# Kernel tuning notes

Measured on AMD Instinct MI355X. Metric: run time of the kernel, lower is better.

## Reference

```python
import jax, jax.numpy as jnp
import numpy as np

B, C, L, E = 65536, 16, 32, 32
EPS = 1e-12

def _normalize(x, axis=-1):
    # F.normalize: x / max(||x||_2, eps)
    n = jnp.sqrt(jnp.sum(x * x, axis=axis, keepdims=True))
    return x / jnp.maximum(n, EPS)

def _linear(x, W, b):
    # torch nn.Linear: y = x @ W.T + b, W: [out, in]
    return jnp.einsum('bcl,el->bce', x, W) + b

def setup_inputs() -> dict:
    key = jax.random.key(0)
    ks = jax.random.split(key, 12)
    s_l = 1.0 / np.sqrt(L)
    s_p1 = 1.0 / np.sqrt(C * E)
    s_p2 = 1.0 / np.sqrt(C * 3)
    return {
        'embed1': jax.random.normal(ks[0], (B, C, L), jnp.float32),
        'embed2': jax.random.normal(ks[1], (B, C, L), jnp.float32),
        'qW': jax.random.uniform(ks[2], (E, L), jnp.float32, -s_l, s_l),
        'qb': jax.random.uniform(ks[3], (E,), jnp.float32, -s_l, s_l),
        'kW': jax.random.uniform(ks[4], (E, L), jnp.float32, -s_l, s_l),
        'kb': jax.random.uniform(ks[5], (E,), jnp.float32, -s_l, s_l),
        'vW': jax.random.uniform(ks[6], (E, L), jnp.float32, -s_l, s_l),
        'vb': jax.random.uniform(ks[7], (E,), jnp.float32, -s_l, s_l),
        'p1W': jax.random.uniform(ks[8], (C * 3, C * E), jnp.float32, -s_p1, s_p1),
        'p1b': jax.random.uniform(ks[9], (C * 3,), jnp.float32, -s_p1, s_p1),
        'p2W': jax.random.uniform(ks[10], (3, C * 3), jnp.float32, -s_p2, s_p2),
        'p2b': jax.random.uniform(ks[11], (3,), jnp.float32, -s_p2, s_p2),
    }

def reference(embed1, embed2, qW, qb, kW, kb, vW, vb, p1W, p1b, p2W, p2b):
    query = _linear(embed1, qW, qb) * _linear(embed2, qW, qb)   # [B,C,E]
    key_t = _linear(embed1, kW, kb) * _linear(embed2, kW, kb)   # [B,C,E]
    value = _linear(embed1, vW, vb) * _linear(embed2, vW, vb)   # [B,C,E]
    attn = jnp.einsum('bce,bde->bcd', _normalize(query), _normalize(key_t))  # [B,C,C]
    # torch F.softmax with dim=None on a 3-D tensor -> legacy dim=0 (batch axis)
    attn = jax.nn.softmax(attn, axis=0)
    # dropout(p=0.2) is identity in eval mode
    out = jnp.einsum('bcd,bce->bde', attn, value)  # attn.transpose(1,2) @ value, [B,C,E]
    h = out.reshape(out.shape[0], -1)              # [B, C*E]
    h = jax.nn.relu(h @ p1W.T + p1b) @ p2W.T + p2b  # [B, 3]
    return _normalize(h)
```

## Files before the change

### kernel.cpp

```cpp
#include <hip/hip_runtime.h>

#define B_TOT 65536
#define WS_P1W 4096
#define WS_EV  (1u << 20)

typedef float f32x4 __attribute__((ext_vector_type(4)));
typedef short s16x8 __attribute__((ext_vector_type(8)));

__device__ __forceinline__ float bf2f(unsigned short h) {
    unsigned u = ((unsigned)h) << 16;
    return __builtin_bit_cast(float, u);
}
__device__ __forceinline__ unsigned pack2(float a, float b) {
    unsigned ua = __builtin_bit_cast(unsigned, a) + 0x8000u;
    unsigned ub = __builtin_bit_cast(unsigned, b) + 0x8000u;
    return __builtin_amdgcn_perm(ub, ua, 0x07060302u);
}
__device__ __forceinline__ unsigned short f2bf(float f) {
    return (unsigned short)((__builtin_bit_cast(unsigned, f) + 0x8000u) >> 16);
}
__device__ __forceinline__ s16x8 cvt8(float4 a, float4 b) {
    uint4 u;
    u.x = pack2(a.x, a.y); u.y = pack2(a.z, a.w);
    u.z = pack2(b.x, b.y); u.w = pack2(b.z, b.w);
    return __builtin_bit_cast(s16x8, u);
}
#define MFMA(a, b, c) __builtin_amdgcn_mfma_f32_16x16x32_bf16((a), (b), (c), 0, 0, 0)

__global__ __launch_bounds__(256) void k0_prep(const float* __restrict__ p1W,
                                               char* __restrict__ ws) {
    int idx = blockIdx.x * 256 + threadIdx.x;
    if (blockIdx.x == 0 && threadIdx.x < 256)
        ((float*)ws)[threadIdx.x] = 0.f;
    int jj   = idx & 7;
    int lane = (idx >> 3) & 63;
    int ktnt = idx >> 9;
    int kt = ktnt & 15, nt = ktnt >> 4;
    int n_lo = lane & 15, q8 = lane >> 4;
    int j  = nt * 16 + n_lo;
    int ip = kt * 32 + q8 * 8 + jj;
    int e_lo = ip >> 5, qq = (ip >> 3) & 3, hh = (ip >> 2) & 1, r = ip & 3;
    int orig = (qq * 4 + r) * 32 + (e_lo + 16 * hh);
    ((unsigned short*)(ws + WS_P1W))[idx] = f2bf(p1W[j * 512 + orig]);
}

__global__ __launch_bounds__(256) void k1_stats(
    const float* __restrict__ e1, const float* __restrict__ e2,
    const float* __restrict__ qW, const float* __restrict__ qb,
    const float* __restrict__ kW, const float* __restrict__ kb,
    const float* __restrict__ vW, const float* __restrict__ vb,
    char* __restrict__ ws) {

    const int tid = threadIdx.x;
    const int lane = tid & 63;
    const int widx = tid >> 6;
    const int col = lane & 15;
    const int quad = lane >> 4;

    __shared__ __align__(16) unsigned short qk_lds[4][2][16 * 40];
    __shared__ float Dblk[256];
    Dblk[tid] = 0.f;
    __syncthreads();

    s16x8 wq[2], wk[2], wv[2];
    f32x4 cbq[2], cbk[2], cbv[2];
    for (int h = 0; h < 2; ++h) {
        int row = col + 16 * h;
        const float4* pq = (const float4*)(qW + row * 32 + quad * 8);
        const float4* pk = (const float4*)(kW + row * 32 + quad * 8);
        const float4* pv = (const float4*)(vW + row * 32 + quad * 8);
        wq[h] = cvt8(pq[0], pq[1]);
        wk[h] = cvt8(pk[0], pk[1]);
        wv[h] = cvt8(pv[0], pv[1]);
        float qv = qb[row], kv = kb[row], vv = vb[row];
        cbq[h] = (f32x4){qv, qv, qv, qv};
        cbk[h] = (f32x4){kv, kv, kv, kv};
        cbv[h] = (f32x4){vv, vv, vv, vv};
    }

    unsigned short* qbuf = qk_lds[widx][0];
    unsigned short* kbuf = qk_lds[widx][1];
    float dacc[4] = {0.f, 0.f, 0.f, 0.f};
    char* evbase = ws + WS_EV;
    const f32x4 z = {0.f, 0.f, 0.f, 0.f};

    const int gw = blockIdx.x * 4 + widx;
    for (int i = 0; i < 8; ++i) {
        const int b = gw * 8 + i;
        const float4* x1p = (const float4*)(e1 + (size_t)b * 512 + col * 32 + quad * 8);
        const float4* x2p = (const float4*)(e2 + (size_t)b * 512 + col * 32 + quad * 8);
        float4 a0 = x1p[0], a1 = x1p[1];
        float4 b0 = x2p[0], b1 = x2p[1];
        s16x8 fx1 = cvt8(a0, a1);
        s16x8 fx2 = cvt8(b0, b1);

        f32x4 q1[2], q2[2], k1[2], k2[2], v1[2], v2[2];
        for (int h = 0; h < 2; ++h) {
            q1[h] = MFMA(fx1, wq[h], cbq[h]); q2[h] = MFMA(fx2, wq[h], cbq[h]);
            k1[h] = MFMA(fx1, wk[h], cbk[h]); k2[h] = MFMA(fx2, wk[h], cbk[h]);
            v1[h] = MFMA(fx1, wv[h], cbv[h]); v2[h] = MFMA(fx2, wv[h], cbv[h]);
        }
        float Qt[2][4], Kt[2][4], Vv[2][4];
        for (int h = 0; h < 2; ++h)
            for (int r = 0; r < 4; ++r) {
                Qt[h][r] = q1[h][r] * q2[h][r];
                Kt[h][r] = k1[h][r] * k2[h][r];
                Vv[h][r] = v1[h][r] * v2[h][r];
            }
        for (int r = 0; r < 4; ++r) {
            int w = (quad * 4 + r) * 20 + col;
            ((unsigned*)qbuf)[w] = pack2(Qt[0][r], Qt[1][r]);
            ((unsigned*)kbuf)[w] = pack2(Kt[0][r], Kt[1][r]);
        }
        s16x8 aq = *(const s16x8*)(qbuf + col * 40 + quad * 8);
        s16x8 bk = *(const s16x8*)(kbuf + col * 40 + quad * 8);
        float qv[8], kv[8], ssq = 0.f, ssk = 0.f;
        for (int j = 0; j < 8; ++j) {
            qv[j] = bf2f((unsigned short)aq[j]); ssq += qv[j] * qv[j];
            kv[j] = bf2f((unsigned short)bk[j]); ssk += kv[j] * kv[j];
        }
        ssq += __shfl_xor(ssq, 16); ssq += __shfl_xor(ssq, 32);
        ssk += __shfl_xor(ssk, 16); ssk += __shfl_xor(ssk, 32);
        float sq = 1.f / fmaxf(sqrtf(ssq), 1e-12f);
        float sk = 1.f / fmaxf(sqrtf(ssk), 1e-12f);
        uint4 uq, uk;
        uq.x = pack2(qv[0] * sq, qv[1] * sq); uq.y = pack2(qv[2] * sq, qv[3] * sq);
        uq.z = pack2(qv[4] * sq, qv[5] * sq); uq.w = pack2(qv[6] * sq, qv[7] * sq);
        uk.x = pack2(kv[0] * sk, kv[1] * sk); uk.y = pack2(kv[2] * sk, kv[3] * sk);
        uk.z = pack2(kv[4] * sk, kv[5] * sk); uk.w = pack2(kv[6] * sk, kv[7] * sk);
        aq = __builtin_bit_cast(s16x8, uq);
        bk = __builtin_bit_cast(s16x8, uk);
        f32x4 S = MFMA(aq, bk, z);

        char* bbase = evbase + (size_t)b * 1536;
        float ex[4];
        for (int r = 0; r < 4; ++r) { ex[r] = __expf(S[r]); dacc[r] += ex[r]; }
        uint2 est; est.x = pack2(ex[0], ex[1]); est.y = pack2(ex[2], ex[3]);
        *(uint2*)(bbase + col * 32 + quad * 8) = est;
        for (int h = 0; h < 2; ++h) {
            uint2 vst;
            vst.x = pack2(Vv[h][0], Vv[h][1]);
            vst.y = pack2(Vv[h][2], Vv[h][3]);
            *(uint2*)(bbase + 512 + ((h * 16 + col) * 2 + (quad >> 1)) * 16 + (quad & 1) * 8) = vst;
        }
    }
    for (int r = 0; r < 4; ++r)
        atomicAdd(&Dblk[col * 16 + quad * 4 + r], dacc[r]);
    __syncthreads();
    atomicAdd(((float*)ws) + tid, Dblk[tid]);
}

__global__ __launch_bounds__(256) void k2_apply(
    const char* __restrict__ ws, const float* __restrict__ p1b,
    const float* __restrict__ p2W, const float* __restrict__ p2b,
    float* __restrict__ out) {

    const int tid = threadIdx.x;
    const int lane = tid & 63;
    const int widx = tid >> 6;
    const int col = lane & 15;
    const int quad = lane >> 4;
    const int qm = quad & 1;

    __shared__ __align__(16) unsigned short Hs[16 * 512];
    float* P = (float*)Hs;

    const float* Dws = (const float*)ws;
    float dinv[8];
    for (int j = 0; j < 8; ++j)
        dinv[j] = 1.f / Dws[col * 16 + qm * 8 + j];

    const char* evbase = ws + WS_EV;
    const unsigned short* p1wp = (const unsigned short*)(ws + WS_P1W);
    const int g = blockIdx.x;
    const f32x4 z = {0.f, 0.f, 0.f, 0.f};
    const s16x8 zz = {0, 0, 0, 0, 0, 0, 0, 0};

    for (int ii = 0; ii < 4; ++ii) {
        const int i = widx * 4 + ii;
        const int b = g * 16 + i;
        const char* bbase = evbase + (size_t)b * 1536;
        s16x8 eraw = *(const s16x8*)(bbase + col * 32 + qm * 16);
        s16x8 bf0 = *(const s16x8*)(bbase + 512 + (col * 2 + qm) * 16);
        s16x8 bf1 = *(const s16x8*)(bbase + 512 + ((16 + col) * 2 + qm) * 16);
        float ef[8];
        for (int j = 0; j < 8; ++j)
            ef[j] = bf2f((unsigned short)eraw[j]) * dinv[j];
        uint4 ua;
        ua.x = pack2(ef[0], ef[1]); ua.y = pack2(ef[2], ef[3]);
        ua.z = pack2(ef[4], ef[5]); ua.w = pack2(ef[6], ef[7]);
        s16x8 afrag = __builtin_bit_cast(s16x8, ua);
        if (quad >= 2) { afrag = zz; bf0 = zz; bf1 = zz; }
        f32x4 o0 = MFMA(afrag, bf0, z);
        f32x4 o1 = MFMA(afrag, bf1, z);
        uint4 uh;
        uh.x = pack2(o0[0], o0[1]); uh.y = pack2(o0[2], o0[3]);
        uh.z = pack2(o1[0], o1[1]); uh.w = pack2(o1[2], o1[3]);
        int chunk = (col * 4 + quad) ^ (i & 7);
        *(uint4*)(Hs + i * 512 + chunk * 8) = uh;
    }
    __syncthreads();

    f32x4 acc[3] = {z, z, z};
    for (int t = 0; t < 4; ++t) {
        int kt = widx * 4 + t;
        int chunk = (kt * 4 + quad) ^ (col & 7);
        s16x8 a = *(const s16x8*)(Hs + col * 512 + chunk * 8);
        for (int nt = 0; nt < 3; ++nt) {
            s16x8 bw = *(const s16x8*)(p1wp + ((nt * 16 + kt) * 64 + lane) * 8);
            acc[nt] = MFMA(a, bw, acc[nt]);
        }
    }
    __syncthreads();

    for (int nt = 0; nt < 3; ++nt)
        *(f32x4*)(P + (widx * 64 + lane) * 12 + nt * 4) = acc[nt];
    __syncthreads();

    if (widx == 0) {
        f32x4 s[3] = {z, z, z};
        for (int w = 0; w < 4; ++w)
            for (int nt = 0; nt < 3; ++nt) {
                f32x4 pv = *(const f32x4*)(P + (w * 64 + lane) * 12 + nt * 4);
                s[nt] += pv;
            }
        float p2w[3][3], p1bias[3];
        for (int nt = 0; nt < 3; ++nt) {
            p1bias[nt] = p1b[col + 16 * nt];
            for (int t = 0; t < 3; ++t) p2w[nt][t] = p2W[t * 48 + col + 16 * nt];
        }
        const float pb0 = p2b[0], pb1 = p2b[1], pb2 = p2b[2];
        float pp[4][3] = {};
        for (int nt = 0; nt < 3; ++nt)
            for (int r = 0; r < 4; ++r) {
                float hv = fmaxf(s[nt][r] + p1bias[nt], 0.f);
                pp[r][0] += hv * p2w[nt][0];
                pp[r][1] += hv * p2w[nt][1];
                pp[r][2] += hv * p2w[nt][2];
            }
        for (int m = 1; m <= 8; m <<= 1)
            for (int r = 0; r < 4; ++r)
                for (int t = 0; t < 3; ++t)
                    pp[r][t] += __shfl_xor(pp[r][t], m);
        for (int r = 0; r < 4; ++r) {
            float h0 = pp[r][0] + pb0, h1 = pp[r][1] + pb1, h2 = pp[r][2] + pb2;
            float inv = 1.f / fmaxf(sqrtf(h0 * h0 + h1 * h1 + h2 * h2), 1e-12f);
            if (col < 3) {
                float v = (col == 0) ? h0 : ((col == 1) ? h1 : h2);
                out[(size_t)(g * 16 + quad * 4 + r) * 3 + col] = v * inv;
            }
        }
    }
}

extern "C" void kernel_launch(void* const* d_in, const int* in_sizes, int n_in,
                              void* d_out, int out_size, void* d_ws, size_t ws_size,
                              hipStream_t stream) {
    const float* e1  = (const float*)d_in[0];
    const float* e2  = (const float*)d_in[1];
    const float* qW  = (const float*)d_in[2];
    const float* qb  = (const float*)d_in[3];
    const float* kW  = (const float*)d_in[4];
    const float* kb  = (const float*)d_in[5];
    const float* vW  = (const float*)d_in[6];
    const float* vb  = (const float*)d_in[7];
    const float* p1W = (const float*)d_in[8];
    const float* p1b = (const float*)d_in[9];
    const float* p2W = (const float*)d_in[10];
    const float* p2b = (const float*)d_in[11];
    float* out = (float*)d_out;
    char* ws = (char*)d_ws;

    k0_prep<<<96, 256, 0, stream>>>(p1W, ws);
    k1_stats<<<2048, 256, 0, stream>>>(e1, e2, qW, qb, kW, kb, vW, vb, ws);
    k2_apply<<<4096, 256, 0, stream>>>(ws, p1b, p2W, p2b, out);
}
```

Before: 342.3 us.

## Replace global atomics with per-block partials, prefetch loads, and split final reduction across warps

```diff
diff --git a/kernel.cpp b/kernel.cpp
--- a/kernel.cpp
+++ b/kernel.cpp
@@ -3,6 +3,8 @@
 #define B_TOT 65536
 #define WS_P1W 4096
 #define WS_EV  (1u << 20)
+#define EV_BYTES 100663296u
+#define WS_PART (WS_EV + EV_BYTES)
 
 typedef float f32x4 __attribute__((ext_vector_type(4)));
 typedef short s16x8 __attribute__((ext_vector_type(8)));
@@ -27,24 +29,7 @@
 }
 #define MFMA(a, b, c) __builtin_amdgcn_mfma_f32_16x16x32_bf16((a), (b), (c), 0, 0, 0)
 
-__global__ __launch_bounds__(256) void k0_prep(const float* __restrict__ p1W,
-                                               char* __restrict__ ws) {
-    int idx = blockIdx.x * 256 + threadIdx.x;
-    if (blockIdx.x == 0 && threadIdx.x < 256)
-        ((float*)ws)[threadIdx.x] = 0.f;
-    int jj   = idx & 7;
-    int lane = (idx >> 3) & 63;
-    int ktnt = idx >> 9;
-    int kt = ktnt & 15, nt = ktnt >> 4;
-    int n_lo = lane & 15, q8 = lane >> 4;
-    int j  = nt * 16 + n_lo;
-    int ip = kt * 32 + q8 * 8 + jj;
-    int e_lo = ip >> 5, qq = (ip >> 3) & 3, hh = (ip >> 2) & 1, r = ip & 3;
-    int orig = (qq * 4 + r) * 32 + (e_lo + 16 * hh);
-    ((unsigned short*)(ws + WS_P1W))[idx] = f2bf(p1W[j * 512 + orig]);
-}
-
-__global__ __launch_bounds__(256) void k1_stats(
+__global__ __launch_bounds__(256, 8) void k1_stats(
     const float* __restrict__ e1, const float* __restrict__ e2,
     const float* __restrict__ qW, const float* __restrict__ qb,
     const float* __restrict__ kW, const float* __restrict__ kb,
@@ -63,7 +48,8 @@
     __syncthreads();
 
     s16x8 wq[2], wk[2], wv[2];
-    f32x4 cbq[2], cbk[2], cbv[2];
+    float bq[2], bk[2], bv[2];
+#pragma unroll
     for (int h = 0; h < 2; ++h) {
         int row = col + 16 * h;
         const float4* pq = (const float4*)(qW + row * 32 + quad * 8);
@@ -72,10 +58,7 @@
         wq[h] = cvt8(pq[0], pq[1]);
         wk[h] = cvt8(pk[0], pk[1]);
         wv[h] = cvt8(pv[0], pv[1]);
-        float qv = qb[row], kv = kb[row], vv = vb[row];
-        cbq[h] = (f32x4){qv, qv, qv, qv};
-        cbk[h] = (f32x4){kv, kv, kv, kv};
-        cbv[h] = (f32x4){vv, vv, vv, vv};
+        bq[h] = qb[row]; bk[h] = kb[row]; bv[h] = vb[row];
     }
 
     unsigned short* qbuf = qk_lds[widx][0];
@@ -85,39 +68,57 @@
     const f32x4 z = {0.f, 0.f, 0.f, 0.f};
 
     const int gw = blockIdx.x * 4 + widx;
+    const float* p1base = e1 + (size_t)gw * 8 * 512 + col * 32 + quad * 8;
+    const float* p2base = e2 + (size_t)gw * 8 * 512 + col * 32 + quad * 8;
+
+    float4 na0 = *(const float4*)(p1base);
+    float4 na1 = *(const float4*)(p1base + 4);
+    float4 nb0 = *(const float4*)(p2base);
+    float4 nb1 = *(const float4*)(p2base + 4);
+
     for (int i = 0; i < 8; ++i) {
         const int b = gw * 8 + i;
-        const float4* x1p = (const float4*)(e1 + (size_t)b * 512 + col * 32 + quad * 8);
-        const float4* x2p = (const float4*)(e2 + (size_t)b * 512 + col * 32 + quad * 8);
-        float4 a0 = x1p[0], a1 = x1p[1];
-        float4 b0 = x2p[0], b1 = x2p[1];
+        float4 a0 = na0, a1 = na1, b0 = nb0, b1 = nb1;
+        if (i < 7) {
+            const float* q1p = p1base + (i + 1) * 512;
+            const float* q2p = p2base + (i + 1) * 512;
+            na0 = *(const float4*)(q1p);
+            na1 = *(const float4*)(q1p + 4);
+            nb0 = *(const float4*)(q2p);
+            nb1 = *(const float4*)(q2p + 4);
+        }
         s16x8 fx1 = cvt8(a0, a1);
         s16x8 fx2 = cvt8(b0, b1);
 
-        f32x4 q1[2], q2[2], k1[2], k2[2], v1[2], v2[2];
+        f32x4 q1v[2], q2v[2], k1v[2], k2v[2], v1v[2], v2v[2];
+#pragma unroll
         for (int h = 0; h < 2; ++h) {
-            q1[h] = MFMA(fx1, wq[h], cbq[h]); q2[h] = MFMA(fx2, wq[h], cbq[h]);
-            k1[h] = MFMA(fx1, wk[h], cbk[h]); k2[h] = MFMA(fx2, wk[h], cbk[h]);
-            v1[h] = MFMA(fx1, wv[h], cbv[h]); v2[h] = MFMA(fx2, wv[h], cbv[h]);
+            q1v[h] = MFMA(fx1, wq[h], z); q2v[h] = MFMA(fx2, wq[h], z);
+            k1v[h] = MFMA(fx1, wk[h], z); k2v[h] = MFMA(fx2, wk[h], z);
+            v1v[h] = MFMA(fx1, wv[h], z); v2v[h] = MFMA(fx2, wv[h], z);
         }
         float Qt[2][4], Kt[2][4], Vv[2][4];
+#pragma unroll
         for (int h = 0; h < 2; ++h)
+#pragma unroll
             for (int r = 0; r < 4; ++r) {
-                Qt[h][r] = q1[h][r] * q2[h][r];
-                Kt[h][r] = k1[h][r] * k2[h][r];
-                Vv[h][r] = v1[h][r] * v2[h][r];
+                Qt[h][r] = (q1v[h][r] + bq[h]) * (q2v[h][r] + bq[h]);
+                Kt[h][r] = (k1v[h][r] + bk[h]) * (k2v[h][r] + bk[h]);
+                Vv[h][r] = (v1v[h][r] + bv[h]) * (v2v[h][r] + bv[h]);
             }
+#pragma unroll
         for (int r = 0; r < 4; ++r) {
             int w = (quad * 4 + r) * 20 + col;
             ((unsigned*)qbuf)[w] = pack2(Qt[0][r], Qt[1][r]);
             ((unsigned*)kbuf)[w] = pack2(Kt[0][r], Kt[1][r]);
         }
         s16x8 aq = *(const s16x8*)(qbuf + col * 40 + quad * 8);
-        s16x8 bk = *(const s16x8*)(kbuf + col * 40 + quad * 8);
+        s16x8 bk8 = *(const s16x8*)(kbuf + col * 40 + quad * 8);
         float qv[8], kv[8], ssq = 0.f, ssk = 0.f;
+#pragma unroll
         for (int j = 0; j < 8; ++j) {
             qv[j] = bf2f((unsigned short)aq[j]); ssq += qv[j] * qv[j];
-            kv[j] = bf2f((unsigned short)bk[j]); ssk += kv[j] * kv[j];
+            kv[j] = bf2f((unsigned short)bk8[j]); ssk += kv[j] * kv[j];
         }
         ssq += __shfl_xor(ssq, 16); ssq += __shfl_xor(ssq, 32);
         ssk += __shfl_xor(ssk, 16); ssk += __shfl_xor(ssk, 32);
@@ -129,14 +130,16 @@
         uk.x = pack2(kv[0] * sk, kv[1] * sk); uk.y = pack2(kv[2] * sk, kv[3] * sk);
         uk.z = pack2(kv[4] * sk, kv[5] * sk); uk.w = pack2(kv[6] * sk, kv[7] * sk);
         aq = __builtin_bit_cast(s16x8, uq);
-        bk = __builtin_bit_cast(s16x8, uk);
-        f32x4 S = MFMA(aq, bk, z);
+        bk8 = __builtin_bit_cast(s16x8, uk);
+        f32x4 S = MFMA(aq, bk8, z);
 
         char* bbase = evbase + (size_t)b * 1536;
         float ex[4];
+#pragma unroll
         for (int r = 0; r < 4; ++r) { ex[r] = __expf(S[r]); dacc[r] += ex[r]; }
         uint2 est; est.x = pack2(ex[0], ex[1]); est.y = pack2(ex[2], ex[3]);
         *(uint2*)(bbase + col * 32 + quad * 8) = est;
+#pragma unroll
         for (int h = 0; h < 2; ++h) {
             uint2 vst;
             vst.x = pack2(Vv[h][0], Vv[h][1]);
@@ -144,10 +147,43 @@
             *(uint2*)(bbase + 512 + ((h * 16 + col) * 2 + (quad >> 1)) * 16 + (quad & 1) * 8) = vst;
         }
     }
+#pragma unroll
     for (int r = 0; r < 4; ++r)
         atomicAdd(&Dblk[col * 16 + quad * 4 + r], dacc[r]);
     __syncthreads();
-    atomicAdd(((float*)ws) + tid, Dblk[tid]);
+    ((float*)(ws + WS_PART))[blockIdx.x * 256 + tid] = Dblk[tid];
+}
+
+__global__ __launch_bounds__(256) void k1b_prep(const float* __restrict__ p1W,
+                                                char* __restrict__ ws) {
+    const int t = threadIdx.x;
+    const int idx = blockIdx.x * 256 + t;
+    if (idx < 24576) {
+        int jj   = idx & 7;
+        int lane = (idx >> 3) & 63;
+        int ktnt = idx >> 9;
+        int kt = ktnt & 15, nt = ktnt >> 4;
+        int n_lo = lane & 15, q8 = lane >> 4;
+        int j2  = nt * 16 + n_lo;
+        int ip  = kt * 32 + q8 * 8 + jj;
+        int e_lo = ip >> 5, qq = (ip >> 3) & 3, hh = (ip >> 2) & 1, r = ip & 3;
+        int orig = (qq * 4 + r) * 32 + (e_lo + 16 * hh);
+        ((unsigned short*)(ws + WS_P1W))[idx] = f2bf(p1W[j2 * 512 + orig]);
+    }
+    const float* part = (const float*)(ws + WS_PART);
+    const int j = blockIdx.x;
+    float s = 0.f;
+#pragma unroll
+    for (int k = 0; k < 8; ++k)
+        s += part[(size_t)(k * 256 + t) * 256 + j];
+    __shared__ float red[256];
+    red[t] = s;
+    __syncthreads();
+    for (int o = 128; o > 0; o >>= 1) {
+        if (t < o) red[t] += red[t + o];
+        __syncthreads();
+    }
+    if (t == 0) ((float*)ws)[j] = 1.f / red[0];
 }
 
 __global__ __launch_bounds__(256) void k2_apply(
@@ -165,10 +201,19 @@
     __shared__ __align__(16) unsigned short Hs[16 * 512];
     float* P = (float*)Hs;
 
+    float p1bias[3], p2w[3][3];
+#pragma unroll
+    for (int nt = 0; nt < 3; ++nt) {
+        p1bias[nt] = p1b[col + 16 * nt];
+#pragma unroll
+        for (int t2 = 0; t2 < 3; ++t2) p2w[nt][t2] = p2W[t2 * 48 + col + 16 * nt];
+    }
+    const float pb0 = p2b[0], pb1 = p2b[1], pb2 = p2b[2];
+
     const float* Dws = (const float*)ws;
-    float dinv[8];
-    for (int j = 0; j < 8; ++j)
-        dinv[j] = 1.f / Dws[col * 16 + qm * 8 + j];
+    const float4 dva = *(const float4*)(Dws + col * 16 + qm * 8);
+    const float4 dvb = *(const float4*)(Dws + col * 16 + qm * 8 + 4);
+    float dinv[8] = {dva.x, dva.y, dva.z, dva.w, dvb.x, dvb.y, dvb.z, dvb.w};
 
     const char* evbase = ws + WS_EV;
     const unsigned short* p1wp = (const unsigned short*)(ws + WS_P1W);
@@ -176,79 +221,99 @@
     const f32x4 z = {0.f, 0.f, 0.f, 0.f};
     const s16x8 zz = {0, 0, 0, 0, 0, 0, 0, 0};
 
-    for (int ii = 0; ii < 4; ++ii) {
-        const int i = widx * 4 + ii;
-        const int b = g * 16 + i;
-        const char* bbase = evbase + (size_t)b * 1536;
-        s16x8 eraw = *(const s16x8*)(bbase + col * 32 + qm * 16);
-        s16x8 bf0 = *(const s16x8*)(bbase + 512 + (col * 2 + qm) * 16);
-        s16x8 bf1 = *(const s16x8*)(bbase + 512 + ((16 + col) * 2 + qm) * 16);
-        float ef[8];
-        for (int j = 0; j < 8; ++j)
-            ef[j] = bf2f((unsigned short)eraw[j]) * dinv[j];
-        uint4 ua;
-        ua.x = pack2(ef[0], ef[1]); ua.y = pack2(ef[2], ef[3]);
-        ua.z = pack2(ef[4], ef[5]); ua.w = pack2(ef[6], ef[7]);
-        s16x8 afrag = __builtin_bit_cast(s16x8, ua);
-        if (quad >= 2) { afrag = zz; bf0 = zz; bf1 = zz; }
-        f32x4 o0 = MFMA(afrag, bf0, z);
-        f32x4 o1 = MFMA(afrag, bf1, z);
-        uint4 uh;
-        uh.x = pack2(o0[0], o0[1]); uh.y = pack2(o0[2], o0[3]);
-        uh.z = pack2(o1[0], o1[1]); uh.w = pack2(o1[2], o1[3]);
-        int chunk = (col * 4 + quad) ^ (i & 7);
-        *(uint4*)(Hs + i * 512 + chunk * 8) = uh;
+    {
+        const char* bb0 = evbase + (size_t)(g * 16 + widx * 4) * 1536;
+        const int eoff  = col * 32 + qm * 16;
+        const int voff0 = 512 + (col * 2 + qm) * 16;
+        const int voff1 = 512 + ((16 + col) * 2 + qm) * 16;
+        s16x8 ne  = *(const s16x8*)(bb0 + eoff);
+        s16x8 nv0 = *(const s16x8*)(bb0 + voff0);
+        s16x8 nv1 = *(const s16x8*)(bb0 + voff1);
+#pragma unroll
+        for (int ii = 0; ii < 4; ++ii) {
+            s16x8 eraw = ne, bf0 = nv0, bf1 = nv1;
+            if (ii < 3) {
+                const char* nb = bb0 + (size_t)(ii + 1) * 1536;
+                ne  = *(const s16x8*)(nb + eoff);
+                nv0 = *(const s16x8*)(nb + voff0);
+                nv1 = *(const s16x8*)(nb + voff1);
+            }
+            float ef[8];
+#pragma unroll
+            for (int j = 0; j < 8; ++j)
+                ef[j] = bf2f((unsigned short)eraw[j]) * dinv[j];
+            uint4 ua;
+            ua.x = pack2(ef[0], ef[1]); ua.y = pack2(ef[2], ef[3]);
+            ua.z = pack2(ef[4], ef[5]); ua.w = pack2(ef[6], ef[7]);
+            s16x8 afrag = __builtin_bit_cast(s16x8, ua);
+            if (quad >= 2) { afrag = zz; bf0 = zz; bf1 = zz; }
+            f32x4 o0 = MFMA(afrag, bf0, z);
+            f32x4 o1 = MFMA(afrag, bf1, z);
+            uint4 uh;
+            uh.x = pack2(o0[0], o0[1]); uh.y = pack2(o0[2], o0[3]);
+            uh.z = pack2(o1[0], o1[1]); uh.w = pack2(o1[2], o1[3]);
+            const int i = widx * 4 + ii;
+            int chunk = (col * 4 + quad) ^ (i & 7);
+            *(uint4*)(Hs + i * 512 + chunk * 8) = uh;
+        }
     }
     __syncthreads();
 
     f32x4 acc[3] = {z, z, z};
-    for (int t = 0; t < 4; ++t) {
-        int kt = widx * 4 + t;
-        int chunk = (kt * 4 + quad) ^ (col & 7);
-        s16x8 a = *(const s16x8*)(Hs + col * 512 + chunk * 8);
-        for (int nt = 0; nt < 3; ++nt) {
-            s16x8 bw = *(const s16x8*)(p1wp + ((nt * 16 + kt) * 64 + lane) * 8);
-            acc[nt] = MFMA(a, bw, acc[nt]);
-        }
-    }
-    __syncthreads();
-
+    {
+        const int kt0 = widx * 4;
+        s16x8 nw0 = *(const s16x8*)(p1wp + ((0 * 16 + kt0) * 64 + lane) * 8);
+        s16x8 nw1 = *(const s16x8*)(p1wp + ((1 * 16 + kt0) * 64 + lane) * 8);
+        s16x8 nw2 = *(const s16x8*)(p1wp + ((2 * 16 + kt0) * 64 + lane) * 8);
+#pragma unroll
+        for (int t2 = 0; t2 < 4; ++t2) {
+            const int kt = widx * 4 + t2;
+            s16x8 w0 = nw0, w1 = nw1, w2 = nw2;
+            if (t2 < 3) {
+                nw0 = *(const s16x8*)(p1wp + ((0 * 16 + kt + 1) * 64 + lane) * 8);
+                nw1 = *(const s16x8*)(p1wp + ((1 * 16 + kt + 1) * 64 + lane) * 8);
+                nw2 = *(const s16x8*)(p1wp + ((2 * 16 + kt + 1) * 64 + lane) * 8);
+            }
+            int chunk = (kt * 4 + quad) ^ (col & 7);
+            s16x8 a = *(const s16x8*)(Hs + col * 512 + chunk * 8);
+            acc[0] = MFMA(a, w0, acc[0]);
+            acc[1] = MFMA(a, w1, acc[1]);
+            acc[2] = MFMA(a, w2, acc[2]);
+        }
+    }
+    __syncthreads();
+
+#pragma unroll
     for (int nt = 0; nt < 3; ++nt)
         *(f32x4*)(P + (widx * 64 + lane) * 12 + nt * 4) = acc[nt];
     __syncthreads();
 
-    if (widx == 0) {
-        f32x4 s[3] = {z, z, z};
+    {
+        float s3[3] = {0.f, 0.f, 0.f};
+#pragma unroll
         for (int w = 0; w < 4; ++w)
-            for (int nt = 0; nt < 3; ++nt) {
-                f32x4 pv = *(const f32x4*)(P + (w * 64 + lane) * 12 + nt * 4);
-                s[nt] += pv;
-            }
-        float p2w[3][3], p1bias[3];
+#pragma unroll
+            for (int nt = 0; nt < 3; ++nt)
+                s3[nt] += P[(w * 64 + lane) * 12 + nt * 4 + widx];
+        float pp[3] = {0.f, 0.f, 0.f};
+#pragma unroll
         for (int nt = 0; nt < 3; ++nt) {
-            p1bias[nt] = p1b[col + 16 * nt];
-            for (int t = 0; t < 3; ++t) p2w[nt][t] = p2W[t * 48 + col + 16 * nt];
-        }
-        const float pb0 = p2b[0], pb1 = p2b[1], pb2 = p2b[2];
-        float pp[4][3] = {};
-        for (int nt = 0; nt < 3; ++nt)
-            for (int r = 0; r < 4; ++r) {
-                float hv = fmaxf(s[nt][r] + p1bias[nt], 0.f);
-                pp[r][0] += hv * p2w[nt][0];
-                pp[r][1] += hv * p2w[nt][1];
-                pp[r][2] += hv * p2w[nt][2];
-            }
-        for (int m = 1; m <= 8; m <<= 1)
-            for (int r = 0; r < 4; ++r)
-                for (int t = 0; t < 3; ++t)
-                    pp[r][t] += __shfl_xor(pp[r][t], m);
-        for (int r = 0; r < 4; ++r) {
-            float h0 = pp[r][0] + pb0, h1 = pp[r][1] + pb1, h2 = pp[r][2] + pb2;
-            float inv = 1.f / fmaxf(sqrtf(h0 * h0 + h1 * h1 + h2 * h2), 1e-12f);
-            if (col < 3) {
-                float v = (col == 0) ? h0 : ((col == 1) ? h1 : h2);
-                out[(size_t)(g * 16 + quad * 4 + r) * 3 + col] = v * inv;
-            }
+            float hv = fmaxf(s3[nt] + p1bias[nt], 0.f);
+            pp[0] += hv * p2w[nt][0];
+            pp[1] += hv * p2w[nt][1];
+            pp[2] += hv * p2w[nt][2];
+        }
+#pragma unroll
+        for (int m = 1; m <= 8; m <<= 1) {
+            pp[0] += __shfl_xor(pp[0], m);
+            pp[1] += __shfl_xor(pp[1], m);
+            pp[2] += __shfl_xor(pp[2], m);
+        }
+        float h0 = pp[0] + pb0, h1 = pp[1] + pb1, h2 = pp[2] + pb2;
+        float inv = 1.f / fmaxf(sqrtf(h0 * h0 + h1 * h1 + h2 * h2), 1e-12f);
+        if (col < 3) {
+            float v = (col == 0) ? h0 : ((col == 1) ? h1 : h2);
+            out[(size_t)(g * 16 + quad * 4 + widx) * 3 + col] = v * inv;
         }
     }
 }
@@ -271,7 +336,7 @@
     float* out = (float*)d_out;
     char* ws = (char*)d_ws;
 
-    k0_prep<<<96, 256, 0, stream>>>(p1W, ws);
     k1_stats<<<2048, 256, 0, stream>>>(e1, e2, qW, qb, kW, kb, vW, vb, ws);
+    k1b_prep<<<256, 256, 0, stream>>>(p1W, ws);
     k2_apply<<<4096, 256, 0, stream>>>(ws, p1b, p2W, p2b, out);
 }
```

Result: slower. 407.1 us (+18.9%).
